# Performance work log

Measured on AMD Instinct MI355X. Metric: run time of the kernel, lower is better.

Reference implementation:

```python
import jax, jax.numpy as jnp
import numpy as np

N, E, IN_F, HID, MSG, OUT, P = 512, 2048, 64, 256, 128, 16, 4
MAX_STEPS = 10 * N  # message cap from the torch while-loop: messages < num_nodes*10


def _lin_init(k, o, i):
    kw, kb = jax.random.split(k)
    s = 1.0 / np.sqrt(i)
    return (jax.random.uniform(kw, (o, i), jnp.float32, -s, s),
            jax.random.uniform(kb, (o,), jnp.float32, -s, s))


def setup_inputs() -> dict:
    key = jax.random.key(0)
    ks = jax.random.split(key, 12)
    xa = jax.random.normal(ks[0], (N, IN_F), jnp.float32)
    first_message = jax.random.normal(ks[1], (N, MSG), jnp.float32)
    edge_index = jax.random.randint(ks[2], (2, E), 0, N, jnp.int32)
    starts = jax.random.randint(ks[3], (N,), 0, 2, jnp.int32)
    enc_W, enc_b = _lin_init(ks[4], HID, IN_F)
    s = 1.0 / np.sqrt(HID)
    W_ih = jax.random.uniform(ks[5], (4 * HID, MSG), jnp.float32, -s, s)
    W_hh = jax.random.uniform(ks[6], (4 * HID, HID), jnp.float32, -s, s)
    b_ih = jax.random.uniform(ks[7], (4 * HID,), jnp.float32, -s, s)
    b_hh = jax.random.uniform(ks[8], (4 * HID,), jnp.float32, -s, s)
    nm_W, nm_b = _lin_init(ks[9], MSG, HID + MSG)
    dec_W = jax.random.uniform(ks[10], (P, OUT, HID), jnp.float32, -s, s)
    dec_b = jax.random.uniform(ks[11], (P, OUT), jnp.float32, -s, s)
    return dict(xa=xa, first_message=first_message, edge_index=edge_index, starts=starts,
                enc_W=enc_W, enc_b=enc_b, W_ih=W_ih, W_hh=W_hh, b_ih=b_ih, b_hh=b_hh,
                nm_W=nm_W, nm_b=nm_b, dec_W=dec_W, dec_b=dec_b)


def _prep_graph(edge_index, starts):
    # Static (non-differentiable) graph preprocessing, mirrors GwACLSTM.neighbors:
    # undirected neighbor *sets*, iterated in sorted order.
    src, dst = np.asarray(edge_index)
    nbr = [set() for _ in range(N)]
    for s, d in zip(src.tolist(), dst.tolist()):
        nbr[s].add(d)
        nbr[d].add(s)
    degs = np.array([len(s) for s in nbr], np.int32)
    maxd = max(1, int(degs.max()))
    nbrs = np.zeros((N, maxd), np.int32)
    for i, s in enumerate(nbr):
        nbrs[i, :len(s)] = sorted(s)
    start_nodes = np.nonzero(np.asarray(starts))[0].astype(np.int32)
    return jnp.asarray(nbrs), jnp.asarray(degs), jnp.asarray(start_nodes), maxd


def _forward(xa, first_message, enc_W, enc_b, W_ih, W_hh, b_ih, b_hh,
             nm_W, nm_b, dec_W, dec_b, nbrs, degs, start_nodes, maxd):
    S0 = int(start_nodes.shape[0])
    cap = S0 + MAX_STEPS * maxd  # queue can never exceed this
    hid = xa @ enc_W.T + enc_b   # per-node initial hidden state = encoder(xa)
    cell = jnp.zeros_like(hid)
    q_nodes = jnp.zeros((cap,), jnp.int32).at[:S0].set(start_nodes)
    q_msgs = jnp.zeros((cap, MSG), xa.dtype)
    if S0 > 0:
        q_msgs = q_msgs.at[:S0, :].set(first_message[start_nodes])

    def step(carry, i):
        q_nodes, q_msgs, hid, cell, t = carry
        node, msg = q_nodes[i], q_msgs[i]
        h_prev, c_prev = hid[node], cell[node]
        # torch.nn.LSTMCell: gates ordered i, f, g, o
        gates = msg @ W_ih.T + b_ih + h_prev @ W_hh.T + b_hh
        gi, gf, gg, go = jnp.split(gates, 4)
        c_new = jax.nn.sigmoid(gf) * c_prev + jax.nn.sigmoid(gi) * jnp.tanh(gg)
        h_new = jax.nn.sigmoid(go) * jnp.tanh(c_new)
        new_msg = jnp.concatenate([h_new, msg]) @ nm_W.T + nm_b
        active = i < t  # queue nonempty
        hid = hid.at[node].set(jnp.where(active, h_new, h_prev))
        cell = cell.at[node].set(jnp.where(active, c_new, c_prev))
        # enqueue new_msg for every neighbor; slots beyond degs[node] are
        # overwritten by later enqueues (tail only advances by degs[node])
        q_nodes = jax.lax.dynamic_update_slice(q_nodes, nbrs[node], (t,))
        q_msgs = jax.lax.dynamic_update_slice(
            q_msgs, jnp.broadcast_to(new_msg, (maxd, MSG)), (t, 0))
        t = jnp.where(active, t + degs[node], t)
        return (q_nodes, q_msgs, hid, cell, t), None

    init = (q_nodes, q_msgs, hid, cell, jnp.int32(S0))
    (_, _, hid, _, _), _ = jax.lax.scan(step, init, jnp.arange(MAX_STEPS, dtype=jnp.int32))
    # graph_class=False: per-node predictions from each decoder head
    logits = jnp.einsum('nh,poh->pno', hid, dec_W) + dec_b[:, None, :]
    return jax.nn.log_softmax(logits, axis=-1)  # [P, N, OUT]


def reference(xa, first_message, edge_index, starts, enc_W, enc_b, W_ih, W_hh,
              b_ih, b_hh, nm_W, nm_b, dec_W, dec_b):
    nbrs, degs, start_nodes, maxd = _prep_graph(edge_index, starts)
    return _forward(xa, first_message, enc_W, enc_b, W_ih, W_hh, b_ih, b_hh,
                    nm_W, nm_b, dec_W, dec_b, nbrs, degs, start_nodes, maxd)
```

## Files before the change

### kernel.cpp

```cpp
#include <hip/hip_runtime.h>
#include <math.h>

#define NN 512
#define EE 2048
#define IN_F 64
#define HID 256
#define MSGD 128
#define OUTC 16
#define MAX_STEPS 5120

#define NWGA 256
#define MAXD 64
#define NCLUS 32
#define WPC 8
#define KSLOT 16

typedef _Float16 h2v __attribute__((ext_vector_type(2)));
typedef _Float16 f16x8 __attribute__((ext_vector_type(8)));
typedef float f32x4 __attribute__((ext_vector_type(4)));

static __device__ __forceinline__ float fdot2u(unsigned int w, unsigned int a, float c) {
    return __builtin_amdgcn_fdot2(__builtin_bit_cast(h2v, w),
                                  __builtin_bit_cast(h2v, a), c, false);
}
static __device__ __forceinline__ unsigned int pkh(float a, float b) {
    h2v h; h.x = (_Float16)a; h.y = (_Float16)b;
    return __builtin_bit_cast(unsigned int, h);
}

__device__ int   g_nbrs64[NN][MAXD];
__device__ int   g_degs[NN];
__device__ int4  g_sched[MAX_STEPS];
__device__ int   g_mready[MAX_STEPS];
__device__ int   g_S0, g_T, g_P;
__device__ int   g_alist[NWGA][MAX_STEPS];
__device__ int   g_acnt[NWGA];
__device__ int   g_noff[NN + 1];
__device__ int   g_nlist[MAX_STEPS];
__device__ int   g_border[NN];
__device__ int   g_nB;
__device__ int   g_tflag[NCLUS][WPC];
__device__ float g_qmsgs[MAX_STEPS][MSGD];
__device__ uint4 g_qmsgP4[MAX_STEPS][16];
__device__ uint4 g_hpk4[2][NN][32];
__device__ float g_hid[NN][HID];
__device__ float g_cell[NN][HID];
__device__ uint4 g_WTph[112 * 512];
__device__ uint4 g_WBm[WPC * 8 * 12 * 64];
__device__ unsigned int g_nmTph[192 * 128];
__device__ float g_bias[1024];

__device__ __forceinline__ float sigm(float x) { return 1.0f / (1.0f + expf(-x)); }

__global__ __launch_bounds__(256) void k_encoder(const float* __restrict__ xa,
                                                 const float* __restrict__ enc_W,
                                                 const float* __restrict__ enc_b) {
    int gid = blockIdx.x * 256 + threadIdx.x;
    int n = gid >> 8, c = gid & 255;
    const float* x = xa + n * IN_F;
    const float* w = enc_W + c * IN_F;
    float acc = enc_b[c];
#pragma unroll 8
    for (int j = 0; j < IN_F; ++j) acc += x[j] * w[j];
    g_hid[n][c] = acc;
    g_cell[n][c] = 0.0f;
}

__device__ __forceinline__ float gw(const float* W_ih, const float* W_hh, int row, int c) {
    return (c < MSGD) ? W_ih[row * MSGD + c] : W_hh[row * HID + (c - MSGD)];
}
__global__ __launch_bounds__(256) void k_prep(const float* __restrict__ W_ih,
                                              const float* __restrict__ W_hh,
                                              const float* __restrict__ b_ih,
                                              const float* __restrict__ b_hh,
                                              const float* __restrict__ nm_W) {
    const int r = blockIdx.x;
    const int t = threadIdx.x;
    for (int q = t; q < 96; q += 256) {
        uint4 v;
        v.x = pkh(gw(W_ih, W_hh, 2 * r, 4 * q),     gw(W_ih, W_hh, 2 * r, 4 * q + 1));
        v.y = pkh(gw(W_ih, W_hh, 2 * r + 1, 4 * q), gw(W_ih, W_hh, 2 * r + 1, 4 * q + 1));
        v.z = pkh(gw(W_ih, W_hh, 2 * r, 4 * q + 2), gw(W_ih, W_hh, 2 * r, 4 * q + 3));
        v.w = pkh(gw(W_ih, W_hh, 2 * r + 1, 4 * q + 2), gw(W_ih, W_hh, 2 * r + 1, 4 * q + 3));
        g_WTph[q * 512 + r] = v;
    }
    if (r < 192 && t < 128)
        g_nmTph[r * 128 + t] = pkh(nm_W[t * 384 + 2 * r], nm_W[t * 384 + 2 * r + 1]);
    if (r == 0)
        for (int g = t; g < 1024; g += 256) g_bias[g] = b_ih[g] + b_hh[g];
}

__global__ __launch_bounds__(64) void k_prepB(const float* __restrict__ W_ih,
                                              const float* __restrict__ W_hh) {
    const int b = blockIdx.x, lane = threadIdx.x;
    const int j = b / 96, rem = b - j * 96;
    const int w = rem / 12, kt = rem - w * 12;
    const int m = lane & 15;
    const int rl = 16 * w + m;
    const int R = (rl >> 5) * 256 + (j << 5) + (rl & 31);
    const int kb = kt * 32 + (lane >> 4) * 8;
    unsigned int d[4];
#pragma unroll
    for (int q = 0; q < 4; ++q)
        d[q] = pkh(gw(W_ih, W_hh, R, kb + 2 * q), gw(W_ih, W_hh, R, kb + 2 * q + 1));
    uint4 v; v.x = d[0]; v.y = d[1]; v.z = d[2]; v.w = d[3];
    g_WBm[((j * 8 + w) * 12 + kt) * 64 + lane] = v;
}

__global__ __launch_bounds__(256) void k_nbr(const int* __restrict__ edge_index) {
    __shared__ unsigned int bits[16];
    const int v = blockIdx.x, tid = threadIdx.x;
    if (tid < 16) bits[tid] = 0u;
    __syncthreads();
    for (int e = tid; e < EE; e += 256) {
        const int s = edge_index[e], d = edge_index[EE + e];
        if (s == v) atomicOr(&bits[d >> 5], 1u << (d & 31));
        if (d == v) atomicOr(&bits[s >> 5], 1u << (s & 31));
    }
    __syncthreads();
    if (tid == 0) {
        int cnt = 0;
        for (int w = 0; w < 16; ++w) {
            unsigned int b = bits[w];
            while (b) {
                const int j = __ffs(b) - 1;
                b &= b - 1u;
                if (cnt < MAXD) g_nbrs64[v][cnt++] = w * 32 + j;
            }
        }
        g_degs[v] = cnt;
    }
}

__global__ __launch_bounds__(1024) void k_sched(const int* __restrict__ starts) {
    __shared__ int s_nx[MAX_STEPS];
    __shared__ int s_ny[MAX_STEPS];
    __shared__ int scanbuf[2][1024];
    __shared__ int s_deg[NN];
    __shared__ int s_off[NN + 1];
    __shared__ int s_csr[4160];
    __shared__ int s_nodes[NN];
    __shared__ int s_cnt[NN];
    __shared__ int s_misc[4];
    __shared__ int s_hist[64];
    const int tid = threadIdx.x;

    const int stt = (tid < NN && starts[tid] != 0) ? 1 : 0;
    const int dg0 = (tid < NN) ? g_degs[tid] : 0;
    if (tid < NN) s_deg[tid] = dg0;
    for (int i = tid; i < MAX_STEPS; i += 1024) s_ny[i] = 0x7fffffff;

    scanbuf[0][tid] = dg0;
    __syncthreads();
    int src = 0;
    for (int off = 1; off < 1024; off <<= 1) {
        int v = scanbuf[src][tid];
        if (tid >= off) v += scanbuf[src][tid - off];
        scanbuf[src ^ 1][tid] = v;
        src ^= 1;
        __syncthreads();
    }
    if (tid <= NN) s_off[tid] = scanbuf[src][tid] - ((tid < NN) ? dg0 : 0);
    __syncthreads();

    scanbuf[0][tid] = stt;
    __syncthreads();
    src = 0;
    for (int off = 1; off < 1024; off <<= 1) {
        int v = scanbuf[src][tid];
        if (tid >= off) v += scanbuf[src][tid - off];
        scanbuf[src ^ 1][tid] = v;
        src ^= 1;
        __syncthreads();
    }
    if (stt) s_nodes[scanbuf[src][tid] - 1] = tid;
    const int S0tot = scanbuf[src][1023];
    __syncthreads();

    if (tid < NN) {
        const int o = s_off[tid], dg = s_deg[tid];
        for (int e = 0; e < dg; ++e) s_csr[o + e] = g_nbrs64[tid][e];
    }
    const int S0 = (S0tot < MAX_STEPS) ? S0tot : MAX_STEPS;
    int known = S0;
    for (int i = tid; i < known; i += 1024) s_nx[i] = s_nodes[i];
    __syncthreads();

    for (int round = 0; round < 8 && known > 0; ++round) {
        const int C = (known + 1023) >> 10;
        const int base = tid * C;
        int lsum = 0;
        for (int j = 0; j < C; ++j) {
            int i = base + j;
            if (i < known) lsum += s_deg[s_nx[i]];
        }
        scanbuf[0][tid] = lsum;
        __syncthreads();
        src = 0;
        for (int off = 1; off < 1024; off <<= 1) {
            int v = scanbuf[src][tid];
            if (tid >= off) v += scanbuf[src][tid - off];
            scanbuf[src ^ 1][tid] = v;
            src ^= 1;
            __syncthreads();
        }
        const int excl = (tid == 0) ? 0 : scanbuf[src][tid - 1];
        const int total = scanbuf[src][1023];
        int t = S0 + excl;
        for (int j = 0; j < C; ++j) {
            int i = base + j;
            if (i < known) {
                const int nd = s_nx[i];
                const int dg = s_deg[nd], o = s_off[nd];
                s_ny[i] = t;
                for (int e = 0; e < dg; ++e) {
                    const int pos = t + e;
                    if (pos >= known && pos < MAX_STEPS) s_nx[pos] = s_csr[o + e];
                }
                t += dg;
            }
        }
        __syncthreads();
        int newknown = S0 + total;
        if (newknown > MAX_STEPS) newknown = MAX_STEPS;
        if (newknown == known) break;
        known = newknown;
    }
    __syncthreads();
    const int kn = known;
    if (tid == 0) s_misc[1] = kn;
    __syncthreads();
    for (int i = tid; i < kn; i += 1024)
        if (s_ny[i] <= i) atomicMin(&s_misc[1], i);
    __syncthreads();
    const int istar = s_misc[1];
    if (tid == 0) s_misc[2] = istar;
    __syncthreads();
    for (int i = tid; i < istar; i += 1024)
        if (s_ny[i] >= istar) atomicMin(&s_misc[2], i);
    __syncthreads();
    const int P = s_misc[2];

    for (int i = tid; i < MAX_STEPS; i += 1024) {
        int4 sc;
        if (i < kn) { sc.x = s_nx[i]; sc.y = s_ny[i]; sc.z = s_deg[sc.x]; }
        else { sc.x = 0; sc.y = 0x7fffffff; sc.z = 0; }
        sc.w = 0;
        g_sched[i] = sc;
    }
    if (tid == 0) { g_S0 = S0; g_T = istar; g_P = P; }

    if (tid < NN) s_cnt[tid] = 0;
    __syncthreads();
    for (int i = P + tid; i < istar; i += 1024) atomicAdd(&s_cnt[s_nx[i]], 1);
    __syncthreads();
    const int cnt0 = (tid < NN) ? s_cnt[tid] : 0;
    scanbuf[0][tid] = cnt0;
    __syncthreads();
    src = 0;
    for (int off = 1; off < 1024; off <<= 1) {
        int v = scanbuf[src][tid];
        if (tid >= off) v += scanbuf[src][tid - off];
        scanbuf[src ^ 1][tid] = v;
        src ^= 1;
        __syncthreads();
    }
    if (tid <= NN) g_noff[tid] = scanbuf[src][tid] - ((tid < NN) ? cnt0 : 0);

    if (tid < 64) s_hist[tid] = 0;
    __syncthreads();
    if (tid < NN && cnt0 > 0) atomicAdd(&s_hist[(cnt0 < 63) ? cnt0 : 63], 1);
    __syncthreads();
    if (tid == 0) {
        int acc = 0;
        for (int b = 63; b >= 1; --b) { const int t = s_hist[b]; s_hist[b] = acc; acc += t; }
        g_nB = acc;
    }
    __syncthreads();
    if (tid < NN && cnt0 > 0) {
        const int p = atomicAdd(&s_hist[(cnt0 < 63) ? cnt0 : 63], 1);
        g_border[p] = tid;
    }
    if (tid < NCLUS * WPC) g_tflag[tid >> 3][tid & 7] = 0;

    for (int i = tid; i < MAX_STEPS; i += 1024) g_mready[i] = (i < S0) ? 1 : 0;
}

__global__ __launch_bounds__(256) void k_lists() {
    __shared__ int sWOff[4];
    __shared__ int sBase;
    const int b = blockIdx.x, tid = threadIdx.x;
    const int lane = tid & 63, wv = tid >> 6;
    if (b < NN) {
        const int v = b;
        const int lo = g_P, hi = g_T;
        if (tid == 0) sBase = g_noff[v];
        __syncthreads();
        for (int st = lo; st < hi; st += 256) {
            const int i = st + tid;
            const bool m = (i < hi) && (g_sched[i].x == v);
            const unsigned long long bal = __ballot(m);
            const int rank = __popcll(bal & ((1ull << lane) - 1ull));
            if (lane == 0) sWOff[wv] = __popcll(bal);
            __syncthreads();
            if (tid == 0) {
                int acc = sBase;
                for (int w = 0; w < 4; ++w) { const int t = sWOff[w]; sWOff[w] = acc; acc += t; }
                sBase = acc;
            }
            __syncthreads();
            if (m) g_nlist[sWOff[wv] + rank] = i;
            __syncthreads();
        }
    } else {
        const int w0 = b - NN;
        const int hi = g_P;
        if (tid == 0) sBase = 0;
        __syncthreads();
        for (int st = 0; st < hi; st += 256) {
            const int i = st + tid;
            const bool m = (i < hi) && ((g_sched[i].x & (NWGA - 1)) == w0);
            const unsigned long long bal = __ballot(m);
            const int rank = __popcll(bal & ((1ull << lane) - 1ull));
            if (lane == 0) sWOff[wv] = __popcll(bal);
            __syncthreads();
            if (tid == 0) {
                int acc = sBase;
                for (int w = 0; w < 4; ++w) { const int t = sWOff[w]; sWOff[w] = acc; acc += t; }
                sBase = acc;
            }
            __syncthreads();
            if (m) g_alist[w0][sWOff[wv] + rank] = i;
            __syncthreads();
        }
        if (tid == 0) g_acnt[w0] = sBase;
    }
}

__global__ __launch_bounds__(128) void k_qinit(const float* __restrict__ first_message) {
    const int i = blockIdx.x;
    if (i >= g_S0) return;
    const int node = g_sched[i].x;
    g_qmsgs[i][threadIdx.x] = first_message[node * MSGD + threadIdx.x];
}

__global__ __launch_bounds__(512, 1) void k_phaseA(const float* __restrict__ nm_b) {
    __shared__ float sAct[MSGD];
    __shared__ float sNH[2][HID], sNC[2][HID];
    __shared__ float sGates[1024];
    __shared__ float sPart[4 * MSGD];
    __shared__ unsigned int sActP[192];
    __shared__ unsigned int sActN[192];
    const int tid = threadIdx.x, wg = blockIdx.x;
    const int cntA = g_acnt[wg];
    if (cntA == 0) return;
    const int S0 = g_S0, T = g_T;
    const float vb0 = g_bias[2 * tid], vb1 = g_bias[2 * tid + 1];
    const uint4* wp = g_WTph + tid;

    for (int idx = tid; idx < 2 * HID; idx += 512) {
        int sl = idx >> 8, u = idx & 255, v = wg + (sl << 8);
        sNH[sl][u] = g_hid[v][u];
        sNC[sl][u] = g_cell[v][u];
    }
    __syncthreads();

    for (int k = 0; k < cntA; ++k) {
        const int s = g_alist[wg][k];
        const int4 sc = g_sched[s];
        const int node = sc.x, y = sc.y, deg = sc.z, sl = node >> 8;
        if (s >= S0) {
            if (tid == 0) {
                while (__hip_atomic_load(&g_mready[s], __ATOMIC_RELAXED,
                                         __HIP_MEMORY_SCOPE_AGENT) == 0)
                    __builtin_amdgcn_s_sleep(2);
            }
            __syncthreads();
            __builtin_amdgcn_fence(__ATOMIC_ACQUIRE, "workgroup");
        }
        if (tid < 64) {
            float a0, a1;
            if (s < S0) { a0 = g_qmsgs[s][2 * tid]; a1 = g_qmsgs[s][2 * tid + 1]; }
            else {
                a0 = __hip_atomic_load(&g_qmsgs[s][2 * tid],     __ATOMIC_RELAXED,
                                       __HIP_MEMORY_SCOPE_AGENT);
                a1 = __hip_atomic_load(&g_qmsgs[s][2 * tid + 1], __ATOMIC_RELAXED,
                                       __HIP_MEMORY_SCOPE_AGENT);
            }
            sAct[2 * tid] = a0; sAct[2 * tid + 1] = a1;
            sActP[tid] = pkh(a0, a1);
        } else if (tid < 192) {
            const int j = tid - 64;
            sActP[tid] = pkh(sNH[sl][2 * j], sNH[sl][2 * j + 1]);
        }
        __syncthreads();
        {
            float acc0 = vb0, acc1 = vb1;
            uint4 wA[8], wB[8];
#pragma unroll
            for (int j = 0; j < 8; ++j) wA[j] = wp[j * 512];
#pragma unroll
            for (int j = 0; j < 8; ++j) wB[j] = wp[(8 + j) * 512];
#pragma unroll 1
            for (int qb = 0; qb < 96; qb += 16) {
#pragma unroll
                for (int j = 0; j < 8; ++j) {
                    const int q = qb + j;
                    const unsigned int a01 = sActP[2 * q], a23 = sActP[2 * q + 1];
                    acc0 = fdot2u(wA[j].x, a01, acc0); acc1 = fdot2u(wA[j].y, a01, acc1);
                    acc0 = fdot2u(wA[j].z, a23, acc0); acc1 = fdot2u(wA[j].w, a23, acc1);
                }
#pragma unroll
                for (int j = 0; j < 8; ++j) wA[j] = wp[(qb + 16 + j) * 512];
#pragma unroll
                for (int j = 0; j < 8; ++j) {
                    const int q = qb + 8 + j;
                    const unsigned int a01 = sActP[2 * q], a23 = sActP[2 * q + 1];
                    acc0 = fdot2u(wB[j].x, a01, acc0); acc1 = fdot2u(wB[j].y, a01, acc1);
                    acc0 = fdot2u(wB[j].z, a23, acc0); acc1 = fdot2u(wB[j].w, a23, acc1);
                }
#pragma unroll
                for (int j = 0; j < 8; ++j) wB[j] = wp[(qb + 24 + j) * 512];
            }
            ((float2*)sGates)[tid] = make_float2(acc0, acc1);
        }
        __syncthreads();
        if (tid < HID) {
            const int u = tid;
            const float gi = sGates[u], gf = sGates[256 + u];
            const float gg = sGates[512 + u], go = sGates[768 + u];
            const float cp = sNC[sl][u];
            const float cn = sigm(gf) * cp + sigm(gi) * tanhf(gg);
            const float hn = sigm(go) * tanhf(cn);
            sNC[sl][u] = cn;
            sNH[sl][u] = hn;
        }
        __syncthreads();
        if (tid < 128) sActN[tid] = pkh(sNH[sl][2 * tid], sNH[sl][2 * tid + 1]);
        else if (tid < 192) {
            const int j = tid - 128;
            sActN[tid] = pkh(sAct[2 * j], sAct[2 * j + 1]);
        }
        __syncthreads();
        {
            const int o = tid & (MSGD - 1), cq = tid >> 7;
            float p = 0.0f;
#pragma unroll 8
            for (int j = 0; j < 48; ++j) {
                const int cp = 48 * cq + j;
                p = fdot2u(g_nmTph[cp * 128 + o], sActN[cp], p);
            }
            sPart[cq * MSGD + o] = p;
        }
        __syncthreads();
        const int lim = (y + deg <= T) ? deg : (T - y);
        if (tid < MSGD) {
            const float m = nm_b[tid] + sPart[tid] + sPart[MSGD + tid]
                          + sPart[2 * MSGD + tid] + sPart[3 * MSGD + tid];
            for (int e = 0; e < lim; ++e)
                __hip_atomic_store(&g_qmsgs[y + e][tid], m, __ATOMIC_RELAXED,
                                   __HIP_MEMORY_SCOPE_AGENT);
        }
        __syncthreads();
        if (tid < lim)
            __hip_atomic_store(&g_mready[y + tid], 1, __ATOMIC_RELAXED,
                               __HIP_MEMORY_SCOPE_AGENT);
    }
    __syncthreads();
    for (int idx = tid; idx < 2 * HID; idx += 512) {
        int sl = idx >> 8, u = idx & 255, v = wg + (sl << 8);
        g_hid[v][u]  = sNH[sl][u];
        g_cell[v][u] = sNC[sl][u];
    }
}

__global__ __launch_bounds__(64) void k_pack() {
    const int b = blockIdx.x, t = threadIdx.x;
    if (b < MAX_STEPS) {
        if (b >= g_P && b < g_T) {
            unsigned int* dst = (unsigned int*)g_qmsgP4[b];
            dst[t] = pkh(g_qmsgs[b][2 * t], g_qmsgs[b][2 * t + 1]);
        }
    } else {
        const int n = b - MAX_STEPS;
        unsigned int* dst = (unsigned int*)g_hpk4[1][n];
        dst[2 * t]     = pkh(g_hid[n][4 * t],     g_hid[n][4 * t + 1]);
        dst[2 * t + 1] = pkh(g_hid[n][4 * t + 2], g_hid[n][4 * t + 3]);
    }
}

__global__ __launch_bounds__(512, 1) void k_phaseB() {
    __shared__ uint4 sB[12 * 64];
    __shared__ float sG[128][17];
    __shared__ float sC[KSLOT][32];
    __shared__ int sNode[KSLOT], sLen[KSLOT], sOff[KSLOT], sStep[KSLOT];
    __shared__ int sMaxLen;
    const int tid = threadIdx.x, wg = blockIdx.x;
    const int c = wg >> 3, j = wg & 7;
    const int wv = tid >> 6, lane = tid & 63;
    const int nB = g_nB;

    if (tid < KSLOT) {
        const int ci = tid * NCLUS + c;
        if (ci < nB) {
            const int v = g_border[ci];
            sNode[tid] = v;
            sOff[tid]  = g_noff[v];
            sLen[tid]  = g_noff[v + 1] - g_noff[v];
        } else { sNode[tid] = -1; sLen[tid] = 0; sOff[tid] = 0; }
    }
    if (tid == 0) sMaxLen = 0;
    __syncthreads();
    if (tid < KSLOT) atomicMax(&sMaxLen, sLen[tid]);
    __syncthreads();
    const int maxlen = sMaxLen;
    if (maxlen == 0) return;

    {
        uint4 z; z.x = z.y = z.z = z.w = 0u;
        for (int i = tid; i < 12 * 64; i += 512) sB[i] = z;
    }
    f16x8 afr[12];
    {
        const f16x8* src = (const f16x8*)g_WBm + ((j * 8 + wv) * 12) * 64 + lane;
#pragma unroll
        for (int kt = 0; kt < 12; ++kt) afr[kt] = src[kt * 64];
    }
    f32x4 bias;
#pragma unroll
    for (int r = 0; r < 4; ++r) {
        const int rl = 16 * wv + (lane >> 4) * 4 + r;
        bias[r] = g_bias[(rl >> 5) * 256 + (j << 5) + (rl & 31)];
    }
    {
        const int k = tid >> 5, u = tid & 31;
        if (sNode[k] >= 0) sC[k][u] = g_cell[sNode[k]][(j << 5) + u];
    }
    __syncthreads();

    for (int tick = 0; tick < maxlen; ++tick) {
        if (tick > 0 && tid < WPC) {
            while (__hip_atomic_load(&g_tflag[c][tid], __ATOMIC_RELAXED,
                                     __HIP_MEMORY_SCOPE_AGENT) < tick)
                __builtin_amdgcn_s_sleep(1);
        }
        if (tid < KSLOT) sStep[tid] = (tick < sLen[tid]) ? g_nlist[sOff[tid] + tick] : -1;
        __syncthreads();
        const int pb = (tick + 1) & 1;
        for (int idx = tid; idx < 12 * 64; idx += 512) {
            const int l = idx & 63, kt = idx >> 6;
            const int n = l & 15, s = sStep[n];
            if (s >= 0) {
                const int g = kt * 4 + (l >> 4);
                uint4 val;
                if (g < 16) {
                    val = g_qmsgP4[s][g];
                } else {
                    const unsigned long long* hp =
                        (const unsigned long long*)g_hpk4[pb][sNode[n]];
                    const unsigned long long lo = __hip_atomic_load(
                        hp + (g - 16) * 2, __ATOMIC_RELAXED, __HIP_MEMORY_SCOPE_AGENT);
                    const unsigned long long hi = __hip_atomic_load(
                        hp + (g - 16) * 2 + 1, __ATOMIC_RELAXED, __HIP_MEMORY_SCOPE_AGENT);
                    val.x = (unsigned int)lo; val.y = (unsigned int)(lo >> 32);
                    val.z = (unsigned int)hi; val.w = (unsigned int)(hi >> 32);
                }
                sB[kt * 64 + l] = val;
            }
        }
        __syncthreads();
        {
            f32x4 acc = bias;
#pragma unroll
            for (int kt = 0; kt < 12; ++kt) {
                const f16x8 bfr = ((const f16x8*)sB)[kt * 64 + lane];
                acc = __builtin_amdgcn_mfma_f32_16x16x32_f16(afr[kt], bfr, acc, 0, 0, 0);
            }
            const int n = lane & 15, rbase = 16 * wv + (lane >> 4) * 4;
#pragma unroll
            for (int r = 0; r < 4; ++r) sG[rbase + r][n] = acc[r];
        }
        __syncthreads();
        {
            const int k = tid >> 5, u = tid & 31;
            const int v = sNode[k];
            const bool act = (sStep[k] >= 0);
            float hn = 0.0f;
            if (act) {
                const float gi = sG[u][k],      gf = sG[32 + u][k];
                const float gg = sG[64 + u][k], go = sG[96 + u][k];
                const float cn = sigm(gf) * sC[k][u] + sigm(gi) * tanhf(gg);
                sC[k][u] = cn;
                hn = sigm(go) * tanhf(cn);
            }
            const float hn1 = __shfl_down(hn, 1);
            if (act) {
                if ((u & 1) == 0) {
                    unsigned int* dst = (unsigned int*)g_hpk4[tick & 1][v];
                    __hip_atomic_store(&dst[(j << 4) + (u >> 1)], pkh(hn, hn1),
                                       __ATOMIC_RELAXED, __HIP_MEMORY_SCOPE_AGENT);
                }
                if (tick == sLen[k] - 1) g_hid[v][(j << 5) + u] = hn;
            }
        }
        __syncthreads();
        if (tid == 0)
            __hip_atomic_store(&g_tflag[c][j], tick + 1, __ATOMIC_RELAXED,
                               __HIP_MEMORY_SCOPE_AGENT);
    }
}

__global__ __launch_bounds__(256) void k_decode(const float* __restrict__ dec_W,
                                                const float* __restrict__ dec_b,
                                                float* __restrict__ out) {
    const int gtid = blockIdx.x * 256 + threadIdx.x;
    const int row = gtid >> 4, lane = gtid & 15;
    const int p = row >> 9, n = row & (NN - 1);
    const float* dw = dec_W + (p * OUTC + lane) * HID;
    float acc = dec_b[p * OUTC + lane];
#pragma unroll 8
    for (int j = 0; j < HID; j += 4) {
        const float4 hv = *(const float4*)&g_hid[n][j];
        const float4 wv = *(const float4*)(dw + j);
        acc += hv.x * wv.x + hv.y * wv.y + hv.z * wv.z + hv.w * wv.w;
    }
    float mx = acc;
    mx = fmaxf(mx, __shfl_xor(mx, 1));
    mx = fmaxf(mx, __shfl_xor(mx, 2));
    mx = fmaxf(mx, __shfl_xor(mx, 4));
    mx = fmaxf(mx, __shfl_xor(mx, 8));
    float s = expf(acc - mx);
    s += __shfl_xor(s, 1);
    s += __shfl_xor(s, 2);
    s += __shfl_xor(s, 4);
    s += __shfl_xor(s, 8);
    out[row * OUTC + lane] = acc - mx - logf(s);
}

extern "C" void kernel_launch(void* const* d_in, const int* in_sizes, int n_in,
                              void* d_out, int out_size, void* d_ws, size_t ws_size,
                              hipStream_t stream) {
    (void)in_sizes; (void)n_in; (void)out_size; (void)d_ws; (void)ws_size;
    const float* xa   = (const float*)d_in[0];
    const float* fm   = (const float*)d_in[1];
    const int*   ei   = (const int*)d_in[2];
    const int*   st   = (const int*)d_in[3];
    const float* encW = (const float*)d_in[4];
    const float* encb = (const float*)d_in[5];
    const float* Wih  = (const float*)d_in[6];
    const float* Whh  = (const float*)d_in[7];
    const float* bih  = (const float*)d_in[8];
    const float* bhh  = (const float*)d_in[9];
    const float* nmW  = (const float*)d_in[10];
    const float* nmb  = (const float*)d_in[11];
    const float* decW = (const float*)d_in[12];
    const float* decb = (const float*)d_in[13];
    float* out = (float*)d_out;

    hipLaunchKernelGGL(k_encoder, dim3(512),       dim3(256),  0, stream, xa, encW, encb);
    hipLaunchKernelGGL(k_prep,    dim3(512),       dim3(256),  0, stream, Wih, Whh, bih, bhh, nmW);
    hipLaunchKernelGGL(k_prepB,   dim3(8 * 8 * 12), dim3(64),  0, stream, Wih, Whh);
    hipLaunchKernelGGL(k_nbr,     dim3(NN),        dim3(256),  0, stream, ei);
    hipLaunchKernelGGL(k_sched,   dim3(1),         dim3(1024), 0, stream, st);
    hipLaunchKernelGGL(k_lists,   dim3(NN + NWGA), dim3(256),  0, stream);
    hipLaunchKernelGGL(k_qinit,   dim3(512),       dim3(128),  0, stream, fm);
    hipLaunchKernelGGL(k_phaseA,  dim3(NWGA),      dim3(512),  0, stream, nmb);
    hipLaunchKernelGGL(k_pack,    dim3(MAX_STEPS + NN), dim3(64), 0, stream);
    hipLaunchKernelGGL(k_phaseB,  dim3(NCLUS * WPC), dim3(512), 0, stream);
    hipLaunchKernelGGL(k_decode,  dim3(128),       dim3(256),  0, stream, decW, decb, out);
}
```

Measured before the change: 240.1 us.

## Split LSTM hidden work across two 1024-thread workgroups per cluster instead of eight

Phase B now gives each node cluster two workgroups of 1024 threads, each owning half of the hidden units, where before eight workgroups of 512 threads each owned a 32-unit slice. Each wave runs two MFMA tiles per step. A workgroup keeps its own half of the packed hidden state in shared memory and only reads the partner's half from a small per-cluster global publish buffer. Each tick now waits on one partner flag instead of eight, and the hidden-state packing in k_pack is folded into phaseB init. This cuts cross-workgroup synchronisation and global traffic per tick, at the cost of fewer workgroups (64 instead of 256) and twice the serial MFMA and gate work per wave.

Result: slower. 291.9 us (+21.5%).

```diff
diff --git a/kernel.cpp b/kernel.cpp
--- a/kernel.cpp
+++ b/kernel.cpp
@@ -12,7 +12,6 @@
 #define NWGA 256
 #define MAXD 64
 #define NCLUS 32
-#define WPC 8
 #define KSLOT 16
 
 typedef _Float16 h2v __attribute__((ext_vector_type(2)));
@@ -39,14 +38,14 @@
 __device__ int   g_nlist[MAX_STEPS];
 __device__ int   g_border[NN];
 __device__ int   g_nB;
-__device__ int   g_tflag[NCLUS][WPC];
+__device__ int   g_tflag2[NCLUS][2];
 __device__ float g_qmsgs[MAX_STEPS][MSGD];
 __device__ uint4 g_qmsgP4[MAX_STEPS][16];
-__device__ uint4 g_hpk4[2][NN][32];
+__device__ uint4 g_hpub[2][NCLUS][2][KSLOT][16];
 __device__ float g_hid[NN][HID];
 __device__ float g_cell[NN][HID];
 __device__ uint4 g_WTph[112 * 512];
-__device__ uint4 g_WBm[WPC * 8 * 12 * 64];
+__device__ uint4 g_WBm[2 * 16 * 2 * 12 * 64];
 __device__ unsigned int g_nmTph[192 * 128];
 __device__ float g_bias[1024];
 
@@ -93,18 +92,18 @@
 __global__ __launch_bounds__(64) void k_prepB(const float* __restrict__ W_ih,
                                               const float* __restrict__ W_hh) {
     const int b = blockIdx.x, lane = threadIdx.x;
-    const int j = b / 96, rem = b - j * 96;
-    const int w = rem / 12, kt = rem - w * 12;
-    const int m = lane & 15;
-    const int rl = 16 * w + m;
-    const int R = (rl >> 5) * 256 + (j << 5) + (rl & 31);
+    const int jj = b / 384, rem = b - jj * 384;
+    const int w = rem / 24, rem2 = rem - w * 24;
+    const int t = rem2 / 12, kt = rem2 - t * 12;
+    const int rl = 32 * w + 16 * t + (lane & 15);
+    const int R = (rl >> 7) * 256 + 128 * jj + (rl & 127);
     const int kb = kt * 32 + (lane >> 4) * 8;
     unsigned int d[4];
 #pragma unroll
     for (int q = 0; q < 4; ++q)
         d[q] = pkh(gw(W_ih, W_hh, R, kb + 2 * q), gw(W_ih, W_hh, R, kb + 2 * q + 1));
     uint4 v; v.x = d[0]; v.y = d[1]; v.z = d[2]; v.w = d[3];
-    g_WBm[((j * 8 + w) * 12 + kt) * 64 + lane] = v;
+    g_WBm[b * 64 + lane] = v;
 }
 
 __global__ __launch_bounds__(256) void k_nbr(const int* __restrict__ edge_index) {
@@ -281,7 +280,7 @@
         const int p = atomicAdd(&s_hist[(cnt0 < 63) ? cnt0 : 63], 1);
         g_border[p] = tid;
     }
-    if (tid < NCLUS * WPC) g_tflag[tid >> 3][tid & 7] = 0;
+    if (tid < NCLUS * 2) g_tflag2[tid >> 1][tid & 1] = -1;
 
     for (int i = tid; i < MAX_STEPS; i += 1024) g_mready[i] = (i < S0) ? 1 : 0;
 }
@@ -476,27 +475,21 @@
 
 __global__ __launch_bounds__(64) void k_pack() {
     const int b = blockIdx.x, t = threadIdx.x;
-    if (b < MAX_STEPS) {
-        if (b >= g_P && b < g_T) {
-            unsigned int* dst = (unsigned int*)g_qmsgP4[b];
-            dst[t] = pkh(g_qmsgs[b][2 * t], g_qmsgs[b][2 * t + 1]);
-        }
-    } else {
-        const int n = b - MAX_STEPS;
-        unsigned int* dst = (unsigned int*)g_hpk4[1][n];
-        dst[2 * t]     = pkh(g_hid[n][4 * t],     g_hid[n][4 * t + 1]);
-        dst[2 * t + 1] = pkh(g_hid[n][4 * t + 2], g_hid[n][4 * t + 3]);
-    }
-}
-
-__global__ __launch_bounds__(512, 1) void k_phaseB() {
+    if (b >= g_P && b < g_T) {
+        unsigned int* dst = (unsigned int*)g_qmsgP4[b];
+        dst[t] = pkh(g_qmsgs[b][2 * t], g_qmsgs[b][2 * t + 1]);
+    }
+}
+
+__global__ __launch_bounds__(1024, 1) void k_phaseB() {
     __shared__ uint4 sB[12 * 64];
-    __shared__ float sG[128][17];
-    __shared__ float sC[KSLOT][32];
+    __shared__ float sG[512][17];
+    __shared__ float sC[KSLOT][128];
+    __shared__ unsigned int hOwn[KSLOT][64];
     __shared__ int sNode[KSLOT], sLen[KSLOT], sOff[KSLOT], sStep[KSLOT];
     __shared__ int sMaxLen;
     const int tid = threadIdx.x, wg = blockIdx.x;
-    const int c = wg >> 3, j = wg & 7;
+    const int c = wg >> 1, jj = wg & 1;
     const int wv = tid >> 6, lane = tid & 63;
     const int nB = g_nB;
 
@@ -518,36 +511,53 @@
 
     {
         uint4 z; z.x = z.y = z.z = z.w = 0u;
-        for (int i = tid; i < 12 * 64; i += 512) sB[i] = z;
-    }
-    f16x8 afr[12];
+        for (int i = tid; i < 12 * 64; i += 1024) sB[i] = z;
+    }
+    f16x8 afr0[12], afr1[12];
     {
-        const f16x8* src = (const f16x8*)g_WBm + ((j * 8 + wv) * 12) * 64 + lane;
-#pragma unroll
-        for (int kt = 0; kt < 12; ++kt) afr[kt] = src[kt * 64];
-    }
-    f32x4 bias;
+        const f16x8* base = (const f16x8*)g_WBm;
+        const int o0 = ((jj * 16 + wv) * 2 + 0) * 12 * 64 + lane;
+        const int o1 = ((jj * 16 + wv) * 2 + 1) * 12 * 64 + lane;
+#pragma unroll
+        for (int kt = 0; kt < 12; ++kt) { afr0[kt] = base[o0 + kt * 64]; afr1[kt] = base[o1 + kt * 64]; }
+    }
+    f32x4 bias0, bias1;
 #pragma unroll
     for (int r = 0; r < 4; ++r) {
-        const int rl = 16 * wv + (lane >> 4) * 4 + r;
-        bias[r] = g_bias[(rl >> 5) * 256 + (j << 5) + (rl & 31)];
-    }
-    {
-        const int k = tid >> 5, u = tid & 31;
-        if (sNode[k] >= 0) sC[k][u] = g_cell[sNode[k]][(j << 5) + u];
-    }
-    __syncthreads();
+        const int rl0 = 32 * wv + (lane >> 4) * 4 + r;
+        const int rl1 = rl0 + 16;
+        bias0[r] = g_bias[(rl0 >> 7) * 256 + 128 * jj + (rl0 & 127)];
+        bias1[r] = g_bias[(rl1 >> 7) * 256 + 128 * jj + (rl1 & 127)];
+    }
+    for (int idx = tid; idx < KSLOT * 128; idx += 1024) {
+        const int k = idx >> 7, u = idx & 127;
+        if (sNode[k] >= 0) sC[k][u] = g_cell[sNode[k]][128 * jj + u];
+    }
+    for (int idx = tid; idx < KSLOT * 64; idx += 1024) {
+        const int k = idx >> 6, d = idx & 63;
+        if (sNode[k] >= 0) {
+            const float h0 = g_hid[sNode[k]][128 * jj + 2 * d];
+            const float h1 = g_hid[sNode[k]][128 * jj + 2 * d + 1];
+            const unsigned int pk = pkh(h0, h1);
+            hOwn[k][d] = pk;
+            __hip_atomic_store((unsigned int*)g_hpub[1][c][jj][k] + d, pk,
+                               __ATOMIC_RELAXED, __HIP_MEMORY_SCOPE_AGENT);
+        }
+    }
+    __syncthreads();
+    if (tid == 0)
+        __hip_atomic_store(&g_tflag2[c][jj], 0, __ATOMIC_RELAXED, __HIP_MEMORY_SCOPE_AGENT);
 
     for (int tick = 0; tick < maxlen; ++tick) {
-        if (tick > 0 && tid < WPC) {
-            while (__hip_atomic_load(&g_tflag[c][tid], __ATOMIC_RELAXED,
+        if (tid == 0) {
+            while (__hip_atomic_load(&g_tflag2[c][jj ^ 1], __ATOMIC_RELAXED,
                                      __HIP_MEMORY_SCOPE_AGENT) < tick)
                 __builtin_amdgcn_s_sleep(1);
         }
         if (tid < KSLOT) sStep[tid] = (tick < sLen[tid]) ? g_nlist[sOff[tid] + tick] : -1;
         __syncthreads();
         const int pb = (tick + 1) & 1;
-        for (int idx = tid; idx < 12 * 64; idx += 512) {
+        for (int idx = tid; idx < 12 * 64; idx += 1024) {
             const int l = idx & 63, kt = idx >> 6;
             const int n = l & 15, s = sStep[n];
             if (s >= 0) {
@@ -556,56 +566,69 @@
                 if (g < 16) {
                     val = g_qmsgP4[s][g];
                 } else {
-                    const unsigned long long* hp =
-                        (const unsigned long long*)g_hpk4[pb][sNode[n]];
-                    const unsigned long long lo = __hip_atomic_load(
-                        hp + (g - 16) * 2, __ATOMIC_RELAXED, __HIP_MEMORY_SCOPE_AGENT);
-                    const unsigned long long hi = __hip_atomic_load(
-                        hp + (g - 16) * 2 + 1, __ATOMIC_RELAXED, __HIP_MEMORY_SCOPE_AGENT);
-                    val.x = (unsigned int)lo; val.y = (unsigned int)(lo >> 32);
-                    val.z = (unsigned int)hi; val.w = (unsigned int)(hi >> 32);
+                    const int gg = g - 16, half = gg >> 4, qi = gg & 15;
+                    if (half == jj) {
+                        val = *(const uint4*)&hOwn[n][qi * 4];
+                    } else {
+                        const unsigned long long* hp =
+                            (const unsigned long long*)g_hpub[pb][c][jj ^ 1][n];
+                        const unsigned long long lo = __hip_atomic_load(
+                            hp + qi * 2, __ATOMIC_RELAXED, __HIP_MEMORY_SCOPE_AGENT);
+                        const unsigned long long hi = __hip_atomic_load(
+                            hp + qi * 2 + 1, __ATOMIC_RELAXED, __HIP_MEMORY_SCOPE_AGENT);
+                        val.x = (unsigned int)lo; val.y = (unsigned int)(lo >> 32);
+                        val.z = (unsigned int)hi; val.w = (unsigned int)(hi >> 32);
+                    }
                 }
                 sB[kt * 64 + l] = val;
             }
         }
         __syncthreads();
         {
-            f32x4 acc = bias;
+            f32x4 acc0 = bias0, acc1 = bias1;
 #pragma unroll
             for (int kt = 0; kt < 12; ++kt) {
                 const f16x8 bfr = ((const f16x8*)sB)[kt * 64 + lane];
-                acc = __builtin_amdgcn_mfma_f32_16x16x32_f16(afr[kt], bfr, acc, 0, 0, 0);
-            }
-            const int n = lane & 15, rbase = 16 * wv + (lane >> 4) * 4;
-#pragma unroll
-            for (int r = 0; r < 4; ++r) sG[rbase + r][n] = acc[r];
+                acc0 = __builtin_amdgcn_mfma_f32_16x16x32_f16(afr0[kt], bfr, acc0, 0, 0, 0);
+                acc1 = __builtin_amdgcn_mfma_f32_16x16x32_f16(afr1[kt], bfr, acc1, 0, 0, 0);
+            }
+            const int n = lane & 15, rbase = 32 * wv + (lane >> 4) * 4;
+#pragma unroll
+            for (int r = 0; r < 4; ++r) {
+                sG[rbase + r][n]      = acc0[r];
+                sG[rbase + 16 + r][n] = acc1[r];
+            }
         }
         __syncthreads();
         {
-            const int k = tid >> 5, u = tid & 31;
+            const int k = tid >> 6, d = tid & 63;
+            const int u0 = 2 * d;
             const int v = sNode[k];
             const bool act = (sStep[k] >= 0);
-            float hn = 0.0f;
             if (act) {
-                const float gi = sG[u][k],      gf = sG[32 + u][k];
-                const float gg = sG[64 + u][k], go = sG[96 + u][k];
-                const float cn = sigm(gf) * sC[k][u] + sigm(gi) * tanhf(gg);
-                sC[k][u] = cn;
-                hn = sigm(go) * tanhf(cn);
-            }
-            const float hn1 = __shfl_down(hn, 1);
-            if (act) {
-                if ((u & 1) == 0) {
-                    unsigned int* dst = (unsigned int*)g_hpk4[tick & 1][v];
-                    __hip_atomic_store(&dst[(j << 4) + (u >> 1)], pkh(hn, hn1),
-                                       __ATOMIC_RELAXED, __HIP_MEMORY_SCOPE_AGENT);
+                float h2[2];
+#pragma unroll
+                for (int e = 0; e < 2; ++e) {
+                    const int u = u0 + e;
+                    const float gi = sG[u][k],       gf = sG[128 + u][k];
+                    const float gg = sG[256 + u][k], go = sG[384 + u][k];
+                    const float cn = sigm(gf) * sC[k][u] + sigm(gi) * tanhf(gg);
+                    sC[k][u] = cn;
+                    h2[e] = sigm(go) * tanhf(cn);
                 }
-                if (tick == sLen[k] - 1) g_hid[v][(j << 5) + u] = hn;
+                const unsigned int pk = pkh(h2[0], h2[1]);
+                hOwn[k][d] = pk;
+                __hip_atomic_store((unsigned int*)g_hpub[tick & 1][c][jj][k] + d, pk,
+                                   __ATOMIC_RELAXED, __HIP_MEMORY_SCOPE_AGENT);
+                if (tick == sLen[k] - 1) {
+                    g_hid[v][128 * jj + u0]     = h2[0];
+                    g_hid[v][128 * jj + u0 + 1] = h2[1];
+                }
             }
         }
         __syncthreads();
         if (tid == 0)
-            __hip_atomic_store(&g_tflag[c][j], tick + 1, __ATOMIC_RELAXED,
+            __hip_atomic_store(&g_tflag2[c][jj], tick + 1, __ATOMIC_RELAXED,
                                __HIP_MEMORY_SCOPE_AGENT);
     }
 }
@@ -659,13 +682,13 @@
 
     hipLaunchKernelGGL(k_encoder, dim3(512),       dim3(256),  0, stream, xa, encW, encb);
     hipLaunchKernelGGL(k_prep,    dim3(512),       dim3(256),  0, stream, Wih, Whh, bih, bhh, nmW);
-    hipLaunchKernelGGL(k_prepB,   dim3(8 * 8 * 12), dim3(64),  0, stream, Wih, Whh);
+    hipLaunchKernelGGL(k_prepB,   dim3(768),       dim3(64),   0, stream, Wih, Whh);
     hipLaunchKernelGGL(k_nbr,     dim3(NN),        dim3(256),  0, stream, ei);
     hipLaunchKernelGGL(k_sched,   dim3(1),         dim3(1024), 0, stream, st);
     hipLaunchKernelGGL(k_lists,   dim3(NN + NWGA), dim3(256),  0, stream);
     hipLaunchKernelGGL(k_qinit,   dim3(512),       dim3(128),  0, stream, fm);
     hipLaunchKernelGGL(k_phaseA,  dim3(NWGA),      dim3(512),  0, stream, nmb);
-    hipLaunchKernelGGL(k_pack,    dim3(MAX_STEPS + NN), dim3(64), 0, stream);
-    hipLaunchKernelGGL(k_phaseB,  dim3(NCLUS * WPC), dim3(512), 0, stream);
+    hipLaunchKernelGGL(k_pack,    dim3(MAX_STEPS), dim3(64),   0, stream);
+    hipLaunchKernelGGL(k_phaseB,  dim3(NCLUS * 2), dim3(1024), 0, stream);
     hipLaunchKernelGGL(k_decode,  dim3(128),       dim3(256),  0, stream, decW, decb, out);
 }
```

## Merge setup kernels and fold packing into phaseA and phaseB

Applied to the files above, without the earlier changes.

Four setup kernels (encoder, weight prep, MFMA weight prep, neighbor build) become one block-partitioned launch, and the queue-init kernel is folded into the lists kernel. The separate pack kernel is removed. Phase A now writes the fp16-packed messages directly, and phase B packs the hidden state for its own slots before setting a ready flag, with flags initialised to -1. The aim is to cut kernel launch count and inter-kernel gaps, at the cost of an extra flag wait at tick 0 and new cross-workgroup ordering assumptions for the packed hidden state.

New measurement: 229.7 us. 4.3% less time.

```diff
diff --git a/kernel.cpp b/kernel.cpp
--- a/kernel.cpp
+++ b/kernel.cpp
@@ -51,84 +51,81 @@
 __device__ float g_bias[1024];
 
 __device__ __forceinline__ float sigm(float x) { return 1.0f / (1.0f + expf(-x)); }
-
-__global__ __launch_bounds__(256) void k_encoder(const float* __restrict__ xa,
-                                                 const float* __restrict__ enc_W,
-                                                 const float* __restrict__ enc_b) {
-    int gid = blockIdx.x * 256 + threadIdx.x;
-    int n = gid >> 8, c = gid & 255;
-    const float* x = xa + n * IN_F;
-    const float* w = enc_W + c * IN_F;
-    float acc = enc_b[c];
-#pragma unroll 8
-    for (int j = 0; j < IN_F; ++j) acc += x[j] * w[j];
-    g_hid[n][c] = acc;
-    g_cell[n][c] = 0.0f;
-}
-
 __device__ __forceinline__ float gw(const float* W_ih, const float* W_hh, int row, int c) {
     return (c < MSGD) ? W_ih[row * MSGD + c] : W_hh[row * HID + (c - MSGD)];
 }
-__global__ __launch_bounds__(256) void k_prep(const float* __restrict__ W_ih,
-                                              const float* __restrict__ W_hh,
-                                              const float* __restrict__ b_ih,
-                                              const float* __restrict__ b_hh,
-                                              const float* __restrict__ nm_W) {
-    const int r = blockIdx.x;
-    const int t = threadIdx.x;
-    for (int q = t; q < 96; q += 256) {
-        uint4 v;
-        v.x = pkh(gw(W_ih, W_hh, 2 * r, 4 * q),     gw(W_ih, W_hh, 2 * r, 4 * q + 1));
-        v.y = pkh(gw(W_ih, W_hh, 2 * r + 1, 4 * q), gw(W_ih, W_hh, 2 * r + 1, 4 * q + 1));
-        v.z = pkh(gw(W_ih, W_hh, 2 * r, 4 * q + 2), gw(W_ih, W_hh, 2 * r, 4 * q + 3));
-        v.w = pkh(gw(W_ih, W_hh, 2 * r + 1, 4 * q + 2), gw(W_ih, W_hh, 2 * r + 1, 4 * q + 3));
-        g_WTph[q * 512 + r] = v;
-    }
-    if (r < 192 && t < 128)
-        g_nmTph[r * 128 + t] = pkh(nm_W[t * 384 + 2 * r], nm_W[t * 384 + 2 * r + 1]);
-    if (r == 0)
-        for (int g = t; g < 1024; g += 256) g_bias[g] = b_ih[g] + b_hh[g];
-}
-
-__global__ __launch_bounds__(64) void k_prepB(const float* __restrict__ W_ih,
-                                              const float* __restrict__ W_hh) {
-    const int b = blockIdx.x, lane = threadIdx.x;
-    const int j = b / 96, rem = b - j * 96;
-    const int w = rem / 12, kt = rem - w * 12;
-    const int m = lane & 15;
-    const int rl = 16 * w + m;
-    const int R = (rl >> 5) * 256 + (j << 5) + (rl & 31);
-    const int kb = kt * 32 + (lane >> 4) * 8;
-    unsigned int d[4];
-#pragma unroll
-    for (int q = 0; q < 4; ++q)
-        d[q] = pkh(gw(W_ih, W_hh, R, kb + 2 * q), gw(W_ih, W_hh, R, kb + 2 * q + 1));
-    uint4 v; v.x = d[0]; v.y = d[1]; v.z = d[2]; v.w = d[3];
-    g_WBm[((j * 8 + w) * 12 + kt) * 64 + lane] = v;
-}
-
-__global__ __launch_bounds__(256) void k_nbr(const int* __restrict__ edge_index) {
-    __shared__ unsigned int bits[16];
-    const int v = blockIdx.x, tid = threadIdx.x;
-    if (tid < 16) bits[tid] = 0u;
-    __syncthreads();
-    for (int e = tid; e < EE; e += 256) {
-        const int s = edge_index[e], d = edge_index[EE + e];
-        if (s == v) atomicOr(&bits[d >> 5], 1u << (d & 31));
-        if (d == v) atomicOr(&bits[s >> 5], 1u << (s & 31));
-    }
-    __syncthreads();
-    if (tid == 0) {
-        int cnt = 0;
-        for (int w = 0; w < 16; ++w) {
-            unsigned int b = bits[w];
-            while (b) {
-                const int j = __ffs(b) - 1;
-                b &= b - 1u;
-                if (cnt < MAXD) g_nbrs64[v][cnt++] = w * 32 + j;
-            }
-        }
-        g_degs[v] = cnt;
+
+__global__ __launch_bounds__(256) void k_setup(const float* __restrict__ xa,
+                                               const float* __restrict__ enc_W,
+                                               const float* __restrict__ enc_b,
+                                               const float* __restrict__ W_ih,
+                                               const float* __restrict__ W_hh,
+                                               const float* __restrict__ b_ih,
+                                               const float* __restrict__ b_hh,
+                                               const float* __restrict__ nm_W,
+                                               const int* __restrict__ edge_index) {
+    const int b = blockIdx.x, tid = threadIdx.x;
+    if (b < 512) {
+        const int gid = b * 256 + tid;
+        const int n = gid >> 8, ccol = gid & 255;
+        const float* x = xa + n * IN_F;
+        const float* w = enc_W + ccol * IN_F;
+        float acc = enc_b[ccol];
+#pragma unroll 8
+        for (int j = 0; j < IN_F; ++j) acc += x[j] * w[j];
+        g_hid[n][ccol] = acc;
+        g_cell[n][ccol] = 0.0f;
+    } else if (b < 1024) {
+        const int r = b - 512;
+        for (int q = tid; q < 96; q += 256) {
+            uint4 v;
+            v.x = pkh(gw(W_ih, W_hh, 2 * r, 4 * q),     gw(W_ih, W_hh, 2 * r, 4 * q + 1));
+            v.y = pkh(gw(W_ih, W_hh, 2 * r + 1, 4 * q), gw(W_ih, W_hh, 2 * r + 1, 4 * q + 1));
+            v.z = pkh(gw(W_ih, W_hh, 2 * r, 4 * q + 2), gw(W_ih, W_hh, 2 * r, 4 * q + 3));
+            v.w = pkh(gw(W_ih, W_hh, 2 * r + 1, 4 * q + 2), gw(W_ih, W_hh, 2 * r + 1, 4 * q + 3));
+            g_WTph[q * 512 + r] = v;
+        }
+        if (r < 192 && tid < 128)
+            g_nmTph[r * 128 + tid] = pkh(nm_W[tid * 384 + 2 * r], nm_W[tid * 384 + 2 * r + 1]);
+        if (r == 0)
+            for (int g = tid; g < 1024; g += 256) g_bias[g] = b_ih[g] + b_hh[g];
+    } else if (b < 1216) {
+        const int b4 = (b - 1024) * 4 + (tid >> 6);
+        const int lane = tid & 63;
+        const int j = b4 / 96, rem = b4 - j * 96;
+        const int w = rem / 12, kt = rem - w * 12;
+        const int rl = 16 * w + (lane & 15);
+        const int R = (rl >> 5) * 256 + (j << 5) + (rl & 31);
+        const int kb = kt * 32 + (lane >> 4) * 8;
+        unsigned int d[4];
+#pragma unroll
+        for (int q = 0; q < 4; ++q)
+            d[q] = pkh(gw(W_ih, W_hh, R, kb + 2 * q), gw(W_ih, W_hh, R, kb + 2 * q + 1));
+        uint4 v; v.x = d[0]; v.y = d[1]; v.z = d[2]; v.w = d[3];
+        g_WBm[b4 * 64 + lane] = v;
+    } else {
+        __shared__ unsigned int bits[16];
+        const int v = b - 1216;
+        if (tid < 16) bits[tid] = 0u;
+        __syncthreads();
+        for (int e = tid; e < EE; e += 256) {
+            const int s = edge_index[e], d = edge_index[EE + e];
+            if (s == v) atomicOr(&bits[d >> 5], 1u << (d & 31));
+            if (d == v) atomicOr(&bits[s >> 5], 1u << (s & 31));
+        }
+        __syncthreads();
+        if (tid == 0) {
+            int cnt = 0;
+            for (int w = 0; w < 16; ++w) {
+                unsigned int bb = bits[w];
+                while (bb) {
+                    const int j = __ffs(bb) - 1;
+                    bb &= bb - 1u;
+                    if (cnt < MAXD) g_nbrs64[v][cnt++] = w * 32 + j;
+                }
+            }
+            g_degs[v] = cnt;
+        }
     }
 }
 
@@ -281,12 +278,12 @@
         const int p = atomicAdd(&s_hist[(cnt0 < 63) ? cnt0 : 63], 1);
         g_border[p] = tid;
     }
-    if (tid < NCLUS * WPC) g_tflag[tid >> 3][tid & 7] = 0;
+    if (tid < NCLUS * WPC) g_tflag[tid >> 3][tid & 7] = -1;
 
     for (int i = tid; i < MAX_STEPS; i += 1024) g_mready[i] = (i < S0) ? 1 : 0;
 }
 
-__global__ __launch_bounds__(256) void k_lists() {
+__global__ __launch_bounds__(256) void k_lists2(const float* __restrict__ first_message) {
     __shared__ int sWOff[4];
     __shared__ int sBase;
     const int b = blockIdx.x, tid = threadIdx.x;
@@ -312,7 +309,7 @@
             if (m) g_nlist[sWOff[wv] + rank] = i;
             __syncthreads();
         }
-    } else {
+    } else if (b < NN + NWGA) {
         const int w0 = b - NN;
         const int hi = g_P;
         if (tid == 0) sBase = 0;
@@ -334,14 +331,11 @@
             __syncthreads();
         }
         if (tid == 0) g_acnt[w0] = sBase;
-    }
-}
-
-__global__ __launch_bounds__(128) void k_qinit(const float* __restrict__ first_message) {
-    const int i = blockIdx.x;
-    if (i >= g_S0) return;
-    const int node = g_sched[i].x;
-    g_qmsgs[i][threadIdx.x] = first_message[node * MSGD + threadIdx.x];
+    } else {
+        const int i = (b - NN - NWGA) * 2 + (tid >> 7);
+        const int col = tid & 127;
+        if (i < g_S0) g_qmsgs[i][col] = first_message[g_sched[i].x * MSGD + col];
+    }
 }
 
 __global__ __launch_bounds__(512, 1) void k_phaseA(const float* __restrict__ nm_b) {
@@ -457,9 +451,15 @@
         if (tid < MSGD) {
             const float m = nm_b[tid] + sPart[tid] + sPart[MSGD + tid]
                           + sPart[2 * MSGD + tid] + sPart[3 * MSGD + tid];
+            const float mN = __shfl_down(m, 1);
             for (int e = 0; e < lim; ++e)
                 __hip_atomic_store(&g_qmsgs[y + e][tid], m, __ATOMIC_RELAXED,
                                    __HIP_MEMORY_SCOPE_AGENT);
+            if ((tid & 1) == 0) {
+                const unsigned int pm = pkh(m, mN);
+                unsigned int* pd = (unsigned int*)g_qmsgP4;
+                for (int e = 0; e < lim; ++e) pd[(y + e) * 64 + (tid >> 1)] = pm;
+            }
         }
         __syncthreads();
         if (tid < lim)
@@ -471,21 +471,6 @@
         int sl = idx >> 8, u = idx & 255, v = wg + (sl << 8);
         g_hid[v][u]  = sNH[sl][u];
         g_cell[v][u] = sNC[sl][u];
-    }
-}
-
-__global__ __launch_bounds__(64) void k_pack() {
-    const int b = blockIdx.x, t = threadIdx.x;
-    if (b < MAX_STEPS) {
-        if (b >= g_P && b < g_T) {
-            unsigned int* dst = (unsigned int*)g_qmsgP4[b];
-            dst[t] = pkh(g_qmsgs[b][2 * t], g_qmsgs[b][2 * t + 1]);
-        }
-    } else {
-        const int n = b - MAX_STEPS;
-        unsigned int* dst = (unsigned int*)g_hpk4[1][n];
-        dst[2 * t]     = pkh(g_hid[n][4 * t],     g_hid[n][4 * t + 1]);
-        dst[2 * t + 1] = pkh(g_hid[n][4 * t + 2], g_hid[n][4 * t + 3]);
     }
 }
 
@@ -536,10 +521,21 @@
         const int k = tid >> 5, u = tid & 31;
         if (sNode[k] >= 0) sC[k][u] = g_cell[sNode[k]][(j << 5) + u];
     }
-    __syncthreads();
+    for (int idx = tid; idx < KSLOT * 16; idx += 512) {
+        const int k = idx >> 4, d = idx & 15;
+        if (sNode[k] >= 0) {
+            const float h0 = g_hid[sNode[k]][(j << 5) + 2 * d];
+            const float h1 = g_hid[sNode[k]][(j << 5) + 2 * d + 1];
+            __hip_atomic_store((unsigned int*)g_hpk4[1][sNode[k]] + (j << 4) + d,
+                               pkh(h0, h1), __ATOMIC_RELAXED, __HIP_MEMORY_SCOPE_AGENT);
+        }
+    }
+    __syncthreads();
+    if (tid == 0)
+        __hip_atomic_store(&g_tflag[c][j], 0, __ATOMIC_RELAXED, __HIP_MEMORY_SCOPE_AGENT);
 
     for (int tick = 0; tick < maxlen; ++tick) {
-        if (tick > 0 && tid < WPC) {
+        if (tid < WPC) {
             while (__hip_atomic_load(&g_tflag[c][tid], __ATOMIC_RELAXED,
                                      __HIP_MEMORY_SCOPE_AGENT) < tick)
                 __builtin_amdgcn_s_sleep(1);
@@ -657,15 +653,11 @@
     const float* decb = (const float*)d_in[13];
     float* out = (float*)d_out;
 
-    hipLaunchKernelGGL(k_encoder, dim3(512),       dim3(256),  0, stream, xa, encW, encb);
-    hipLaunchKernelGGL(k_prep,    dim3(512),       dim3(256),  0, stream, Wih, Whh, bih, bhh, nmW);
-    hipLaunchKernelGGL(k_prepB,   dim3(8 * 8 * 12), dim3(64),  0, stream, Wih, Whh);
-    hipLaunchKernelGGL(k_nbr,     dim3(NN),        dim3(256),  0, stream, ei);
-    hipLaunchKernelGGL(k_sched,   dim3(1),         dim3(1024), 0, stream, st);
-    hipLaunchKernelGGL(k_lists,   dim3(NN + NWGA), dim3(256),  0, stream);
-    hipLaunchKernelGGL(k_qinit,   dim3(512),       dim3(128),  0, stream, fm);
-    hipLaunchKernelGGL(k_phaseA,  dim3(NWGA),      dim3(512),  0, stream, nmb);
-    hipLaunchKernelGGL(k_pack,    dim3(MAX_STEPS + NN), dim3(64), 0, stream);
-    hipLaunchKernelGGL(k_phaseB,  dim3(NCLUS * WPC), dim3(512), 0, stream);
-    hipLaunchKernelGGL(k_decode,  dim3(128),       dim3(256),  0, stream, decW, decb, out);
-}
+    hipLaunchKernelGGL(k_setup,  dim3(1728),            dim3(256),  0, stream,
+                       xa, encW, encb, Wih, Whh, bih, bhh, nmW, ei);
+    hipLaunchKernelGGL(k_sched,  dim3(1),               dim3(1024), 0, stream, st);
+    hipLaunchKernelGGL(k_lists2, dim3(NN + NWGA + 256), dim3(256),  0, stream, fm);
+    hipLaunchKernelGGL(k_phaseA, dim3(NWGA),            dim3(512),  0, stream, nmb);
+    hipLaunchKernelGGL(k_phaseB, dim3(NCLUS * WPC),     dim3(512),  0, stream);
+    hipLaunchKernelGGL(k_decode, dim3(128),             dim3(256),  0, stream, decW, decb, out);
+}
```
